# Kernel tuning notes

Measured on AMD Instinct MI355X. Metric: run time of the kernel, lower is better.

## Reference

```python
import jax, jax.numpy as jnp
import numpy as np

BN_EPS = 1e-5
NN_EPS = 1e-8

def _bn_relu(h, gamma, beta):
    # training-mode BatchNorm1d over (B, L) per channel, biased variance
    mean = jnp.mean(h, axis=(0, 2), keepdims=True)
    var = jnp.mean((h - mean) ** 2, axis=(0, 2), keepdims=True)
    hn = (h - mean) * jax.lax.rsqrt(var + BN_EPS)
    return jax.nn.relu(hn * gamma[None, :, None] + beta[None, :, None])

def setup_inputs() -> dict:
    key = jax.random.key(0)
    ks = jax.random.split(key, 8)
    B, N, M, Cin, Cout = 2, 2048, 8192, 512, 256
    return {
        "x1": jax.random.normal(ks[0], (B, N, Cin), jnp.float32),
        "p1": jax.random.uniform(ks[1], (B, N, 3), jnp.float32),
        "x2": jax.random.normal(ks[2], (B, M, Cout), jnp.float32),
        "p2": jax.random.uniform(ks[3], (B, M, 3), jnp.float32),
        "W_up": jax.random.normal(ks[4], (Cout, Cin), jnp.float32) * (1.0 / np.sqrt(Cin)),
        "gamma_up": jnp.ones((Cout,), jnp.float32),
        "beta_up": jnp.zeros((Cout,), jnp.float32),
        "W_lat": jax.random.normal(ks[5], (Cout, Cout), jnp.float32) * (1.0 / np.sqrt(Cout)),
        "gamma_lat": jnp.ones((Cout,), jnp.float32),
        "beta_lat": jnp.zeros((Cout,), jnp.float32),
    }

def reference(x1, p1, x2, p2, W_up, gamma_up, beta_up, W_lat, gamma_lat, beta_lat):
    B, M, _ = p2.shape
    # up_mlp: 1x1 conv (bias=False) + BN + ReLU -> (B, Cout, N)
    h1 = _bn_relu(jnp.einsum('bnc,oc->bon', x1, W_up), gamma_up, beta_up)
    # three_nn: squared distances from each p2 query to all p1 points
    d2 = (jnp.sum(p2 ** 2, -1)[:, :, None] + jnp.sum(p1 ** 2, -1)[:, None, :]
          - 2.0 * jnp.einsum('bmd,bnd->bmn', p2, p1))  # (B, M, N)
    neg_d, idx = jax.lax.top_k(-d2, 3)                 # 3 smallest squared dists
    dist = -neg_d                                      # (B, M, 3)
    dist_recip = 1.0 / (dist + NN_EPS)
    weight = dist_recip / jnp.sum(dist_recip, axis=2, keepdims=True)  # (B, M, 3)
    # three_interpolate: weighted gather of h1 along point axis
    C = h1.shape[1]
    g = jnp.take_along_axis(h1, idx.reshape(B, 1, M * 3), axis=2).reshape(B, C, M, 3)
    interp = jnp.einsum('bcmk,bmk->bcm', g, weight)    # (B, Cout, M)
    # lateral_mlp on x2
    h2 = _bn_relu(jnp.einsum('bmc,oc->bom', x2, W_lat), gamma_lat, beta_lat)
    y = interp + h2                                    # (B, Cout, M)
    return jnp.transpose(y, (0, 2, 1)), p2             # (B, M, Cout), (B, M, 3)
```

## Files before the change

### kernel.cpp

```cpp
#include <hip/hip_runtime.h>

#define BATCH 2
#define NPTS  2048
#define MPTS  8192
#define CIN1  512
#define CIN2  256
#define COUT  256
#define ROWS1 (BATCH*NPTS)
#define ROWS2 (BATCH*MPTS)
#define BN_EPS 1e-5f
#define NN_EPS 1e-8f

#define NCHUNK 16
#define CHUNK  (NPTS / NCHUNK)

typedef __attribute__((ext_vector_type(8))) short  bf16x8;
typedef __attribute__((ext_vector_type(4))) float  f32x4;

__device__ __forceinline__ unsigned short bf16_rne(float x) {
    unsigned u = __float_as_uint(x);
    u += 0x7FFFu + ((u >> 16) & 1u);
    return (unsigned short)(u >> 16);
}
__device__ __forceinline__ float bf16_f32(unsigned short h) {
    return __uint_as_float(((unsigned)h) << 16);
}
__device__ __forceinline__ void split2(float x, unsigned short& h, unsigned short& l) {
    h = bf16_rne(x);
    l = bf16_rne(x - bf16_f32(h));
}

template<int K, int BM, int BN>
__global__ __launch_bounds__(256)
void gemm_mfma(const float* __restrict__ A, const float* __restrict__ W,
               float* __restrict__ C, float* __restrict__ stats) {
    constexpr int BK = 32;
    constexpr int LDK = 40;
    constexpr int WM = BM / 2, WN = BN / 2;
    constexpr int FM = WM / 16, FN = WN / 16;
    __shared__ unsigned short Ah[BM][LDK], Al[BM][LDK];
    __shared__ unsigned short Bh[BN][LDK], Bl[BN][LDK];
    __shared__ float red[BN][8];

    const int tid = threadIdx.x;
    const int m0 = blockIdx.y * BM;
    const int o0 = blockIdx.x * BN;
    const int lane = tid & 63, wid = tid >> 6;
    const int wy = wid >> 1, wx = wid & 1;
    const int lr = lane & 15, lg = lane >> 4;
    const int srow = tid >> 3;
    const int squad = (tid & 7) * 4;

    f32x4 acc[FM][FN];
    #pragma unroll
    for (int i = 0; i < FM; ++i)
        #pragma unroll
        for (int j = 0; j < FN; ++j)
            acc[i][j] = (f32x4){0.f, 0.f, 0.f, 0.f};

    const float* Abase = A + (size_t)m0 * K + squad;
    const float* Wbase = W + (size_t)o0 * K + squad;

    for (int k0 = 0; k0 < K; k0 += BK) {
        __syncthreads();
        #pragma unroll
        for (int r = srow; r < BM; r += 32) {
            float4 v = *(const float4*)(Abase + (size_t)r * K + k0);
            ushort4 h, l;
            split2(v.x, h.x, l.x); split2(v.y, h.y, l.y);
            split2(v.z, h.z, l.z); split2(v.w, h.w, l.w);
            *(ushort4*)&Ah[r][squad] = h;
            *(ushort4*)&Al[r][squad] = l;
        }
        #pragma unroll
        for (int r = srow; r < BN; r += 32) {
            float4 v = *(const float4*)(Wbase + (size_t)r * K + k0);
            ushort4 h, l;
            split2(v.x, h.x, l.x); split2(v.y, h.y, l.y);
            split2(v.z, h.z, l.z); split2(v.w, h.w, l.w);
            *(ushort4*)&Bh[r][squad] = h;
            *(ushort4*)&Bl[r][squad] = l;
        }
        __syncthreads();

        bf16x8 fah[FM], fal[FM], fbh[FN], fbl[FN];
        #pragma unroll
        for (int i = 0; i < FM; ++i) {
            const int row = wy * WM + i * 16 + lr;
            fah[i] = *(const bf16x8*)&Ah[row][lg * 8];
            fal[i] = *(const bf16x8*)&Al[row][lg * 8];
        }
        #pragma unroll
        for (int j = 0; j < FN; ++j) {
            const int row = wx * WN + j * 16 + lr;
            fbh[j] = *(const bf16x8*)&Bh[row][lg * 8];
            fbl[j] = *(const bf16x8*)&Bl[row][lg * 8];
        }
        #pragma unroll
        for (int i = 0; i < FM; ++i)
            #pragma unroll
            for (int j = 0; j < FN; ++j) {
                acc[i][j] = __builtin_amdgcn_mfma_f32_16x16x32_bf16(fah[i], fbh[j], acc[i][j], 0, 0, 0);
                acc[i][j] = __builtin_amdgcn_mfma_f32_16x16x32_bf16(fal[i], fbh[j], acc[i][j], 0, 0, 0);
                acc[i][j] = __builtin_amdgcn_mfma_f32_16x16x32_bf16(fah[i], fbl[j], acc[i][j], 0, 0, 0);
            }
    }

    #pragma unroll
    for (int i = 0; i < FM; ++i)
        #pragma unroll
        for (int j = 0; j < FN; ++j) {
            const int col = o0 + wx * WN + j * 16 + lr;
            const int rbase = m0 + wy * WM + i * 16 + lg * 4;
            #pragma unroll
            for (int r = 0; r < 4; ++r)
                C[(size_t)(rbase + r) * COUT + col] = acc[i][j][r];
        }

    #pragma unroll
    for (int j = 0; j < FN; ++j) {
        float s = 0.f;
        #pragma unroll
        for (int i = 0; i < FM; ++i)
            #pragma unroll
            for (int r = 0; r < 4; ++r)
                s += acc[i][j][r];
        red[wx * WN + j * 16 + lr][wy * 4 + lg] = s;
    }
    __syncthreads();
    if (tid < BN) {
        float s = 0.f;
        #pragma unroll
        for (int k = 0; k < 8; ++k) s += red[tid][k];
        atomicAdd(&stats[o0 + tid], s);
    }
    __syncthreads();
    #pragma unroll
    for (int j = 0; j < FN; ++j) {
        float q = 0.f;
        #pragma unroll
        for (int i = 0; i < FM; ++i)
            #pragma unroll
            for (int r = 0; r < 4; ++r)
                q = fmaf(acc[i][j][r], acc[i][j][r], q);
        red[wx * WN + j * 16 + lr][wy * 4 + lg] = q;
    }
    __syncthreads();
    if (tid < BN) {
        float q = 0.f;
        #pragma unroll
        for (int k = 0; k < 8; ++k) q += red[tid][k];
        atomicAdd(&stats[COUT + o0 + tid], q);
    }
}

__global__ __launch_bounds__(256)
void three_nn_part(const float* __restrict__ p1, const float* __restrict__ p2,
                   float2* __restrict__ part) {
    __shared__ float4 pts[CHUNK];
    const int b = blockIdx.z;
    const int c = blockIdx.y;
    const int t = threadIdx.x;
    const int n0 = c * CHUNK;
    if (t < CHUNK) {
        const float* P1 = p1 + ((size_t)b * NPTS + n0) * 3;
        float x = P1[t * 3 + 0], y = P1[t * 3 + 1], z = P1[t * 3 + 2];
        pts[t] = make_float4(x, y, z, x * x + y * y + z * z);
    }
    __syncthreads();
    const int m = blockIdx.x * 256 + t;
    const float* q = p2 + ((size_t)b * MPTS + m) * 3;
    const float qx = q[0], qy = q[1], qz = q[2];
    const float s2 = qx * qx + qy * qy + qz * qz;
    float d0 = 1e30f, d1 = 1e30f, d2 = 1e30f;
    int   i0 = 0,     i1 = 0,     i2 = 0;
    #pragma unroll 4
    for (int n = 0; n < CHUNK; ++n) {
        float4 p = pts[n];
        float dot = p.x * qx + p.y * qy + p.z * qz;
        float d = s2 + p.w - 2.0f * dot;
        if (d < d2) {
            if (d < d1) {
                d2 = d1; i2 = i1;
                if (d < d0) { d1 = d0; i1 = i0; d0 = d; i0 = n0 + n; }
                else        { d1 = d;  i1 = n0 + n; }
            } else { d2 = d; i2 = n0 + n; }
        }
    }
    float2* o = part + ((size_t)(b * MPTS + m) * NCHUNK + c) * 3;
    o[0] = make_float2(d0, __int_as_float(i0));
    o[1] = make_float2(d1, __int_as_float(i1));
    o[2] = make_float2(d2, __int_as_float(i2));
}

__global__ __launch_bounds__(256)
void three_nn_merge(const float2* __restrict__ part,
                    int* __restrict__ idx, float* __restrict__ wgt) {
    const int row = blockIdx.x * 256 + threadIdx.x;
    const float4* pp = (const float4*)(part + (size_t)row * NCHUNK * 3);
    float d0 = 1e30f, d1 = 1e30f, d2 = 1e30f;
    int   i0 = 0,     i1 = 0,     i2 = 0;
    #pragma unroll
    for (int j = 0; j < NCHUNK * 3 / 2; ++j) {
        float4 v = pp[j];
        #pragma unroll
        for (int h = 0; h < 2; ++h) {
            float d = h ? v.z : v.x;
            int   i = __float_as_int(h ? v.w : v.y);
            if (d < d2) {
                if (d < d1) {
                    d2 = d1; i2 = i1;
                    if (d < d0) { d1 = d0; i1 = i0; d0 = d; i0 = i; }
                    else        { d1 = d;  i1 = i; }
                } else { d2 = d; i2 = i; }
            }
        }
    }
    const float r0 = 1.0f / (d0 + NN_EPS);
    const float r1 = 1.0f / (d1 + NN_EPS);
    const float r2 = 1.0f / (d2 + NN_EPS);
    const float rs = r0 + r1 + r2;
    const size_t o = (size_t)row * 3;
    idx[o + 0] = i0; idx[o + 1] = i1; idx[o + 2] = i2;
    wgt[o + 0] = r0 / rs; wgt[o + 1] = r1 / rs; wgt[o + 2] = r2 / rs;
}

__global__ __launch_bounds__(256)
void final_combine(const float* __restrict__ h1, const float* __restrict__ stats,
                   const float* __restrict__ g1, const float* __restrict__ b1,
                   const float* __restrict__ g2, const float* __restrict__ b2,
                   const int* __restrict__ idx, const float* __restrict__ wgt,
                   float* __restrict__ out) {
    const int c = threadIdx.x;
    const int row = blockIdx.x;
    const int b = row >> 13;
    const float inv1 = 1.0f / (float)ROWS1;
    const float mean1 = stats[c] * inv1;
    const float var1  = fmaf(-mean1, mean1, stats[COUT + c] * inv1);
    const float sc1   = g1[c] / sqrtf(var1 + BN_EPS);
    const float sh1   = fmaf(-mean1, sc1, b1[c]);
    const float inv2 = 1.0f / (float)ROWS2;
    const float mean2 = stats[512 + c] * inv2;
    const float var2  = fmaf(-mean2, mean2, stats[768 + c] * inv2);
    const float sc2   = g2[c] / sqrtf(var2 + BN_EPS);
    const float sh2   = fmaf(-mean2, sc2, b2[c]);

    const size_t o3 = (size_t)row * 3;
    const int i0 = idx[o3 + 0], i1 = idx[o3 + 1], i2 = idx[o3 + 2];
    const float w0 = wgt[o3 + 0], w1 = wgt[o3 + 1], w2 = wgt[o3 + 2];
    const float* hb = h1 + (size_t)b * NPTS * COUT;
    const float v0 = fmaxf(fmaf(hb[(size_t)i0 * COUT + c], sc1, sh1), 0.f);
    const float v1 = fmaxf(fmaf(hb[(size_t)i1 * COUT + c], sc1, sh1), 0.f);
    const float v2 = fmaxf(fmaf(hb[(size_t)i2 * COUT + c], sc1, sh1), 0.f);
    const float g = w0 * v0 + w1 * v1 + w2 * v2;

    const size_t oi = (size_t)row * COUT + c;
    const float y = fmaxf(fmaf(out[oi], sc2, sh2), 0.f);
    out[oi] = y + g;
}

extern "C" void kernel_launch(void* const* d_in, const int* in_sizes, int n_in,
                              void* d_out, int out_size, void* d_ws, size_t ws_size,
                              hipStream_t stream) {
    const float* x1       = (const float*)d_in[0];
    const float* p1       = (const float*)d_in[1];
    const float* x2       = (const float*)d_in[2];
    const float* p2       = (const float*)d_in[3];
    const float* W_up     = (const float*)d_in[4];
    const float* gamma_up = (const float*)d_in[5];
    const float* beta_up  = (const float*)d_in[6];
    const float* W_lat    = (const float*)d_in[7];
    const float* gamma_lat= (const float*)d_in[8];
    const float* beta_lat = (const float*)d_in[9];
    float* out = (float*)d_out;

    float*  h1    = (float*)d_ws;
    float*  stats = h1 + (size_t)ROWS1 * COUT;
    int*    idx   = (int*)(stats + 1024);
    float*  wgt   = (float*)(idx + (size_t)ROWS2 * 3);
    float2* part  = (float2*)(wgt + (size_t)ROWS2 * 3);

    hipMemsetAsync(stats, 0, 1024 * sizeof(float), stream);

    gemm_mfma<CIN1, 64, 64><<<dim3(COUT / 64, ROWS1 / 64), 256, 0, stream>>>(
        x1, W_up, h1, stats);

    gemm_mfma<CIN2, 128, 128><<<dim3(COUT / 128, ROWS2 / 128), 256, 0, stream>>>(
        x2, W_lat, out, stats + 512);

    three_nn_part<<<dim3(MPTS / 256, NCHUNK, BATCH), 256, 0, stream>>>(p1, p2, part);
    three_nn_merge<<<ROWS2 / 256, 256, 0, stream>>>(part, idx, wgt);

    final_combine<<<ROWS2, 256, 0, stream>>>(h1, stats, gamma_up, beta_up,
                                             gamma_lat, beta_lat, idx, wgt, out);

    hipMemcpyAsync(out + (size_t)ROWS2 * COUT, p2,
                   (size_t)ROWS2 * 3 * sizeof(float),
                   hipMemcpyDeviceToDevice, stream);
}
```

Baseline: 198.1 us.

## Split-K the up GEMM with atomics, shrink lateral GEMM tiles, vectorize combine

The up-projection GEMM now splits K four ways and accumulates into a zeroed h1 buffer with float atomics. Its BN statistics move to a separate column-sum kernel, because partial tiles cannot produce them. The lateral GEMM switches from 128x128 to 64x64 tiles so more blocks run at once. final_combine now handles four rows per block with float4 loads and stores. The changes aim to raise occupancy on the small GEMMs and cut per-thread overhead in the gather, at the cost of an extra memset, atomic traffic, an extra kernel pass over h1, and nondeterministic summation order.

```diff
diff --git a/kernel.cpp b/kernel.cpp
--- a/kernel.cpp
+++ b/kernel.cpp
@@ -30,76 +30,73 @@
     l = bf16_rne(x - bf16_f32(h));
 }
 
-template<int K, int BM, int BN>
-__global__ __launch_bounds__(256)
-void gemm_mfma(const float* __restrict__ A, const float* __restrict__ W,
-               float* __restrict__ C, float* __restrict__ stats) {
+template<int K, int KSPLIT, bool FUSE_STATS>
+__global__ __launch_bounds__(256)
+void gemm_mfma64(const float* __restrict__ A, const float* __restrict__ W,
+                 float* __restrict__ C, float* __restrict__ stats) {
     constexpr int BK = 32;
     constexpr int LDK = 40;
-    constexpr int WM = BM / 2, WN = BN / 2;
-    constexpr int FM = WM / 16, FN = WN / 16;
-    __shared__ unsigned short Ah[BM][LDK], Al[BM][LDK];
-    __shared__ unsigned short Bh[BN][LDK], Bl[BN][LDK];
-    __shared__ float red[BN][8];
+    constexpr int KCH = K / KSPLIT;
+    __shared__ unsigned short Ah[64][LDK], Al[64][LDK];
+    __shared__ unsigned short Bh[64][LDK], Bl[64][LDK];
+    __shared__ float red[64][8];
 
     const int tid = threadIdx.x;
-    const int m0 = blockIdx.y * BM;
-    const int o0 = blockIdx.x * BN;
+    const int m0 = blockIdx.y * 64;
+    const int o0 = blockIdx.x * 64;
+    const int kbase = blockIdx.z * KCH;
     const int lane = tid & 63, wid = tid >> 6;
     const int wy = wid >> 1, wx = wid & 1;
     const int lr = lane & 15, lg = lane >> 4;
     const int srow = tid >> 3;
     const int squad = (tid & 7) * 4;
 
-    f32x4 acc[FM][FN];
+    f32x4 acc[2][2];
     #pragma unroll
-    for (int i = 0; i < FM; ++i)
-        #pragma unroll
-        for (int j = 0; j < FN; ++j)
+    for (int i = 0; i < 2; ++i)
+        #pragma unroll
+        for (int j = 0; j < 2; ++j)
             acc[i][j] = (f32x4){0.f, 0.f, 0.f, 0.f};
 
-    const float* Abase = A + (size_t)m0 * K + squad;
-    const float* Wbase = W + (size_t)o0 * K + squad;
-
-    for (int k0 = 0; k0 < K; k0 += BK) {
-        __syncthreads();
-        #pragma unroll
-        for (int r = srow; r < BM; r += 32) {
-            float4 v = *(const float4*)(Abase + (size_t)r * K + k0);
+    const float* Abase = A + (size_t)m0 * K + kbase + squad;
+    const float* Wbase = W + (size_t)o0 * K + kbase + squad;
+
+    for (int k0 = 0; k0 < KCH; k0 += BK) {
+        __syncthreads();
+        #pragma unroll
+        for (int rr = 0; rr < 2; ++rr) {
+            const int r = srow + rr * 32;
+            float4 va = *(const float4*)(Abase + (size_t)r * K + k0);
+            float4 vb = *(const float4*)(Wbase + (size_t)r * K + k0);
             ushort4 h, l;
-            split2(v.x, h.x, l.x); split2(v.y, h.y, l.y);
-            split2(v.z, h.z, l.z); split2(v.w, h.w, l.w);
+            split2(va.x, h.x, l.x); split2(va.y, h.y, l.y);
+            split2(va.z, h.z, l.z); split2(va.w, h.w, l.w);
             *(ushort4*)&Ah[r][squad] = h;
             *(ushort4*)&Al[r][squad] = l;
-        }
-        #pragma unroll
-        for (int r = srow; r < BN; r += 32) {
-            float4 v = *(const float4*)(Wbase + (size_t)r * K + k0);
-            ushort4 h, l;
-            split2(v.x, h.x, l.x); split2(v.y, h.y, l.y);
-            split2(v.z, h.z, l.z); split2(v.w, h.w, l.w);
+            split2(vb.x, h.x, l.x); split2(vb.y, h.y, l.y);
+            split2(vb.z, h.z, l.z); split2(vb.w, h.w, l.w);
             *(ushort4*)&Bh[r][squad] = h;
             *(ushort4*)&Bl[r][squad] = l;
         }
         __syncthreads();
 
-        bf16x8 fah[FM], fal[FM], fbh[FN], fbl[FN];
-        #pragma unroll
-        for (int i = 0; i < FM; ++i) {
-            const int row = wy * WM + i * 16 + lr;
+        bf16x8 fah[2], fal[2], fbh[2], fbl[2];
+        #pragma unroll
+        for (int i = 0; i < 2; ++i) {
+            const int row = wy * 32 + i * 16 + lr;
             fah[i] = *(const bf16x8*)&Ah[row][lg * 8];
             fal[i] = *(const bf16x8*)&Al[row][lg * 8];
         }
         #pragma unroll
-        for (int j = 0; j < FN; ++j) {
-            const int row = wx * WN + j * 16 + lr;
+        for (int j = 0; j < 2; ++j) {
+            const int row = wx * 32 + j * 16 + lr;
             fbh[j] = *(const bf16x8*)&Bh[row][lg * 8];
             fbl[j] = *(const bf16x8*)&Bl[row][lg * 8];
         }
         #pragma unroll
-        for (int i = 0; i < FM; ++i)
-            #pragma unroll
-            for (int j = 0; j < FN; ++j) {
+        for (int i = 0; i < 2; ++i)
+            #pragma unroll
+            for (int j = 0; j < 2; ++j) {
                 acc[i][j] = __builtin_amdgcn_mfma_f32_16x16x32_bf16(fah[i], fbh[j], acc[i][j], 0, 0, 0);
                 acc[i][j] = __builtin_amdgcn_mfma_f32_16x16x32_bf16(fal[i], fbh[j], acc[i][j], 0, 0, 0);
                 acc[i][j] = __builtin_amdgcn_mfma_f32_16x16x32_bf16(fah[i], fbl[j], acc[i][j], 0, 0, 0);
@@ -107,51 +104,72 @@
     }
 
     #pragma unroll
-    for (int i = 0; i < FM; ++i)
-        #pragma unroll
-        for (int j = 0; j < FN; ++j) {
-            const int col = o0 + wx * WN + j * 16 + lr;
-            const int rbase = m0 + wy * WM + i * 16 + lg * 4;
-            #pragma unroll
-            for (int r = 0; r < 4; ++r)
-                C[(size_t)(rbase + r) * COUT + col] = acc[i][j][r];
-        }
-
-    #pragma unroll
-    for (int j = 0; j < FN; ++j) {
-        float s = 0.f;
-        #pragma unroll
-        for (int i = 0; i < FM; ++i)
-            #pragma unroll
-            for (int r = 0; r < 4; ++r)
-                s += acc[i][j][r];
-        red[wx * WN + j * 16 + lr][wy * 4 + lg] = s;
-    }
-    __syncthreads();
-    if (tid < BN) {
-        float s = 0.f;
-        #pragma unroll
-        for (int k = 0; k < 8; ++k) s += red[tid][k];
-        atomicAdd(&stats[o0 + tid], s);
-    }
-    __syncthreads();
-    #pragma unroll
-    for (int j = 0; j < FN; ++j) {
-        float q = 0.f;
-        #pragma unroll
-        for (int i = 0; i < FM; ++i)
-            #pragma unroll
-            for (int r = 0; r < 4; ++r)
-                q = fmaf(acc[i][j][r], acc[i][j][r], q);
-        red[wx * WN + j * 16 + lr][wy * 4 + lg] = q;
-    }
-    __syncthreads();
-    if (tid < BN) {
-        float q = 0.f;
-        #pragma unroll
-        for (int k = 0; k < 8; ++k) q += red[tid][k];
-        atomicAdd(&stats[COUT + o0 + tid], q);
-    }
+    for (int i = 0; i < 2; ++i)
+        #pragma unroll
+        for (int j = 0; j < 2; ++j) {
+            const int col = o0 + wx * 32 + j * 16 + lr;
+            const int rbase = m0 + wy * 32 + i * 16 + lg * 4;
+            #pragma unroll
+            for (int r = 0; r < 4; ++r) {
+                if (KSPLIT > 1)
+                    atomicAdd(&C[(size_t)(rbase + r) * COUT + col], acc[i][j][r]);
+                else
+                    C[(size_t)(rbase + r) * COUT + col] = acc[i][j][r];
+            }
+        }
+
+    if constexpr (FUSE_STATS) {
+        #pragma unroll
+        for (int j = 0; j < 2; ++j) {
+            float s = 0.f;
+            #pragma unroll
+            for (int i = 0; i < 2; ++i)
+                #pragma unroll
+                for (int r = 0; r < 4; ++r)
+                    s += acc[i][j][r];
+            red[wx * 32 + j * 16 + lr][wy * 4 + lg] = s;
+        }
+        __syncthreads();
+        if (tid < 64) {
+            float s = 0.f;
+            #pragma unroll
+            for (int k = 0; k < 8; ++k) s += red[tid][k];
+            atomicAdd(&stats[o0 + tid], s);
+        }
+        __syncthreads();
+        #pragma unroll
+        for (int j = 0; j < 2; ++j) {
+            float q = 0.f;
+            #pragma unroll
+            for (int i = 0; i < 2; ++i)
+                #pragma unroll
+                for (int r = 0; r < 4; ++r)
+                    q = fmaf(acc[i][j][r], acc[i][j][r], q);
+            red[wx * 32 + j * 16 + lr][wy * 4 + lg] = q;
+        }
+        __syncthreads();
+        if (tid < 64) {
+            float q = 0.f;
+            #pragma unroll
+            for (int k = 0; k < 8; ++k) q += red[tid][k];
+            atomicAdd(&stats[COUT + o0 + tid], q);
+        }
+    }
+}
+
+__global__ __launch_bounds__(256)
+void colsum256(const float* __restrict__ X, int rowsPerBlock,
+               float* __restrict__ out) {
+    const int c = threadIdx.x;
+    const int r0 = blockIdx.x * rowsPerBlock;
+    float s = 0.f, q = 0.f;
+    for (int r = 0; r < rowsPerBlock; ++r) {
+        float v = X[(size_t)(r0 + r) * COUT + c];
+        s += v;
+        q = fmaf(v, v, q);
+    }
+    atomicAdd(&out[c], s);
+    atomicAdd(&out[COUT + c], q);
 }
 
 __global__ __launch_bounds__(256)
@@ -231,32 +249,62 @@
                    const float* __restrict__ g2, const float* __restrict__ b2,
                    const int* __restrict__ idx, const float* __restrict__ wgt,
                    float* __restrict__ out) {
-    const int c = threadIdx.x;
-    const int row = blockIdx.x;
+    const int t = threadIdx.x;
+    const int row = blockIdx.x * 4 + (t >> 6);
+    const int c = (t & 63) * 4;
     const int b = row >> 13;
-    const float inv1 = 1.0f / (float)ROWS1;
-    const float mean1 = stats[c] * inv1;
-    const float var1  = fmaf(-mean1, mean1, stats[COUT + c] * inv1);
-    const float sc1   = g1[c] / sqrtf(var1 + BN_EPS);
-    const float sh1   = fmaf(-mean1, sc1, b1[c]);
-    const float inv2 = 1.0f / (float)ROWS2;
-    const float mean2 = stats[512 + c] * inv2;
-    const float var2  = fmaf(-mean2, mean2, stats[768 + c] * inv2);
-    const float sc2   = g2[c] / sqrtf(var2 + BN_EPS);
-    const float sh2   = fmaf(-mean2, sc2, b2[c]);
+
+    const float4 sum1 = *(const float4*)&stats[c];
+    const float4 sq1  = *(const float4*)&stats[COUT + c];
+    const float4 sum2 = *(const float4*)&stats[512 + c];
+    const float4 sq2  = *(const float4*)&stats[768 + c];
+    const float4 gg1  = *(const float4*)&g1[c];
+    const float4 bb1  = *(const float4*)&b1[c];
+    const float4 gg2  = *(const float4*)&g2[c];
+    const float4 bb2  = *(const float4*)&b2[c];
+
+    const float inv1 = 1.0f / (float)ROWS1, inv2 = 1.0f / (float)ROWS2;
+    float4 sc1, sh1, sc2, sh2;
+    {
+        float m, v;
+        m = sum1.x*inv1; v = fmaf(-m,m,sq1.x*inv1); sc1.x = gg1.x/sqrtf(v+BN_EPS); sh1.x = fmaf(-m,sc1.x,bb1.x);
+        m = sum1.y*inv1; v = fmaf(-m,m,sq1.y*inv1); sc1.y = gg1.y/sqrtf(v+BN_EPS); sh1.y = fmaf(-m,sc1.y,bb1.y);
+        m = sum1.z*inv1; v = fmaf(-m,m,sq1.z*inv1); sc1.z = gg1.z/sqrtf(v+BN_EPS); sh1.z = fmaf(-m,sc1.z,bb1.z);
+        m = sum1.w*inv1; v = fmaf(-m,m,sq1.w*inv1); sc1.w = gg1.w/sqrtf(v+BN_EPS); sh1.w = fmaf(-m,sc1.w,bb1.w);
+        m = sum2.x*inv2; v = fmaf(-m,m,sq2.x*inv2); sc2.x = gg2.x/sqrtf(v+BN_EPS); sh2.x = fmaf(-m,sc2.x,bb2.x);
+        m = sum2.y*inv2; v = fmaf(-m,m,sq2.y*inv2); sc2.y = gg2.y/sqrtf(v+BN_EPS); sh2.y = fmaf(-m,sc2.y,bb2.y);
+        m = sum2.z*inv2; v = fmaf(-m,m,sq2.z*inv2); sc2.z = gg2.z/sqrtf(v+BN_EPS); sh2.z = fmaf(-m,sc2.z,bb2.z);
+        m = sum2.w*inv2; v = fmaf(-m,m,sq2.w*inv2); sc2.w = gg2.w/sqrtf(v+BN_EPS); sh2.w = fmaf(-m,sc2.w,bb2.w);
+    }
 
     const size_t o3 = (size_t)row * 3;
     const int i0 = idx[o3 + 0], i1 = idx[o3 + 1], i2 = idx[o3 + 2];
     const float w0 = wgt[o3 + 0], w1 = wgt[o3 + 1], w2 = wgt[o3 + 2];
-    const float* hb = h1 + (size_t)b * NPTS * COUT;
-    const float v0 = fmaxf(fmaf(hb[(size_t)i0 * COUT + c], sc1, sh1), 0.f);
-    const float v1 = fmaxf(fmaf(hb[(size_t)i1 * COUT + c], sc1, sh1), 0.f);
-    const float v2 = fmaxf(fmaf(hb[(size_t)i2 * COUT + c], sc1, sh1), 0.f);
-    const float g = w0 * v0 + w1 * v1 + w2 * v2;
+    const float* hb = h1 + (size_t)b * NPTS * COUT + c;
+    const float4 h0 = *(const float4*)(hb + (size_t)i0 * COUT);
+    const float4 h4 = *(const float4*)(hb + (size_t)i1 * COUT);
+    const float4 h8 = *(const float4*)(hb + (size_t)i2 * COUT);
 
     const size_t oi = (size_t)row * COUT + c;
-    const float y = fmaxf(fmaf(out[oi], sc2, sh2), 0.f);
-    out[oi] = y + g;
+    float4 yv = *(const float4*)&out[oi];
+    float4 r;
+    r.x = fmaxf(fmaf(yv.x, sc2.x, sh2.x), 0.f)
+        + w0 * fmaxf(fmaf(h0.x, sc1.x, sh1.x), 0.f)
+        + w1 * fmaxf(fmaf(h4.x, sc1.x, sh1.x), 0.f)
+        + w2 * fmaxf(fmaf(h8.x, sc1.x, sh1.x), 0.f);
+    r.y = fmaxf(fmaf(yv.y, sc2.y, sh2.y), 0.f)
+        + w0 * fmaxf(fmaf(h0.y, sc1.y, sh1.y), 0.f)
+        + w1 * fmaxf(fmaf(h4.y, sc1.y, sh1.y), 0.f)
+        + w2 * fmaxf(fmaf(h8.y, sc1.y, sh1.y), 0.f);
+    r.z = fmaxf(fmaf(yv.z, sc2.z, sh2.z), 0.f)
+        + w0 * fmaxf(fmaf(h0.z, sc1.z, sh1.z), 0.f)
+        + w1 * fmaxf(fmaf(h4.z, sc1.z, sh1.z), 0.f)
+        + w2 * fmaxf(fmaf(h8.z, sc1.z, sh1.z), 0.f);
+    r.w = fmaxf(fmaf(yv.w, sc2.w, sh2.w), 0.f)
+        + w0 * fmaxf(fmaf(h0.w, sc1.w, sh1.w), 0.f)
+        + w1 * fmaxf(fmaf(h4.w, sc1.w, sh1.w), 0.f)
+        + w2 * fmaxf(fmaf(h8.w, sc1.w, sh1.w), 0.f);
+    *(float4*)&out[oi] = r;
 }
 
 extern "C" void kernel_launch(void* const* d_in, const int* in_sizes, int n_in,
@@ -281,18 +329,20 @@
     float2* part  = (float2*)(wgt + (size_t)ROWS2 * 3);
 
     hipMemsetAsync(stats, 0, 1024 * sizeof(float), stream);
-
-    gemm_mfma<CIN1, 64, 64><<<dim3(COUT / 64, ROWS1 / 64), 256, 0, stream>>>(
-        x1, W_up, h1, stats);
-
-    gemm_mfma<CIN2, 128, 128><<<dim3(COUT / 128, ROWS2 / 128), 256, 0, stream>>>(
+    hipMemsetAsync(h1, 0, (size_t)ROWS1 * COUT * sizeof(float), stream);
+
+    gemm_mfma64<CIN1, 4, false><<<dim3(COUT / 64, ROWS1 / 64, 4), 256, 0, stream>>>(
+        x1, W_up, h1, nullptr);
+    colsum256<<<256, 256, 0, stream>>>(h1, ROWS1 / 256, stats);
+
+    gemm_mfma64<CIN2, 1, true><<<dim3(COUT / 64, ROWS2 / 64, 1), 256, 0, stream>>>(
         x2, W_lat, out, stats + 512);
 
     three_nn_part<<<dim3(MPTS / 256, NCHUNK, BATCH), 256, 0, stream>>>(p1, p2, part);
     three_nn_merge<<<ROWS2 / 256, 256, 0, stream>>>(part, idx, wgt);
 
-    final_combine<<<ROWS2, 256, 0, stream>>>(h1, stats, gamma_up, beta_up,
-                                             gamma_lat, beta_lat, idx, wgt, out);
+    final_combine<<<ROWS2 / 4, 256, 0, stream>>>(h1, stats, gamma_up, beta_up,
+                                                 gamma_lat, beta_lat, idx, wgt, out);
 
     hipMemcpyAsync(out + (size_t)ROWS2 * COUT, p2,
                    (size_t)ROWS2 * 3 * sizeof(float),
```

Result: faster. 179.7 us (-9.2%).
